# Performance work log

Hardware: AMD Instinct MI355X
Metric: run time of the kernel (lower is better)

## Reference

```python
import jax, jax.numpy as jnp
import numpy as np

N_CELL, N_WELL = 200000, 512
E_CC, E_CW = 1600000, 65536
CF, WF, ED, H = 12, 8, 1, 64
NEG_SLOPE = 0.2


def _p(k, shape, fan_in):
    return jax.random.normal(k, shape, jnp.float32) * (1.0 / np.sqrt(fan_in))


def setup_inputs() -> dict:
    key = jax.random.key(0)
    ks = jax.random.split(key, 32)
    d = {}
    d['cell_x'] = jax.random.normal(ks[0], (N_CELL, CF), jnp.float32)
    d['well_x'] = jax.random.normal(ks[1], (N_WELL, WF), jnp.float32)
    d['c2c_edge_attr'] = jax.random.normal(ks[2], (E_CC, ED), jnp.float32)
    d['c2c_edge_index'] = jax.random.randint(ks[3], (2, E_CC), 0, N_CELL)
    cw_src = jax.random.randint(ks[4], (E_CW,), 0, N_CELL)
    cw_dst = jax.random.randint(ks[5], (E_CW,), 0, N_WELL)
    d['c2w_edge_index'] = jnp.stack([cw_src, cw_dst])
    d['W_cell_emb'] = _p(ks[6], (CF, H), CF)
    d['b_cell_emb'] = jnp.zeros((H,), jnp.float32)
    d['W_well_emb'] = _p(ks[7], (WF, H), WF)
    d['b_well_emb'] = jnp.zeros((H,), jnp.float32)
    d['W_edge_emb'] = _p(ks[8], (ED, H), ED)
    d['b_edge_emb'] = jnp.zeros((H,), jnp.float32)
    d['conv_lin'] = _p(ks[9], (3, H, H), H)
    d['conv_lin_edge'] = _p(ks[10], (3, H, H), H)
    d['conv_att_src'] = _p(ks[11], (3, H), H)
    d['conv_att_dst'] = _p(ks[12], (3, H), H)
    d['conv_att_edge'] = _p(ks[13], (3, H), H)
    d['conv_bias'] = jnp.zeros((3, H), jnp.float32)
    d['wc_lin'] = _p(ks[14], (H, H), H)
    d['wc_att_src'] = _p(ks[15], (H,), H)
    d['wc_att_dst'] = _p(ks[16], (H,), H)
    d['wc_bias'] = jnp.zeros((H,), jnp.float32)
    d['mlp_W1'] = _p(ks[17], (H, H), H)
    d['mlp_b1'] = jnp.zeros((H,), jnp.float32)
    d['mlp_W2'] = _p(ks[18], (H, 75), H)
    d['mlp_b2'] = jnp.zeros((75,), jnp.float32)
    return d


def segment_softmax(logits, seg, num_segments):
    m = jax.ops.segment_max(logits, seg, num_segments=num_segments)
    m = jnp.where(jnp.isfinite(m), m, 0.0)  # empty segments -> 0
    e = jnp.exp(logits - m[seg])
    s = jax.ops.segment_sum(e, seg, num_segments=num_segments)
    return e / s[seg]


def gat_layer(h_src, h_dst, src, dst, lin, att_s, att_d, bias, num_dst,
              edge_feat=None, lin_edge=None, att_e=None):
    # PyG GATConv, heads=1, concat=False, add_self_loops=False
    hs = h_src @ lin                      # [Ns, H]
    hd = hs if h_dst is h_src else h_dst @ lin
    alpha = (hs @ att_s)[src] + (hd @ att_d)[dst]  # [E]
    if edge_feat is not None:
        alpha = alpha + (edge_feat @ lin_edge) @ att_e
    alpha = jax.nn.leaky_relu(alpha, NEG_SLOPE)
    p = segment_softmax(alpha, dst, num_dst)       # scatter-softmax per dst
    out = jax.ops.segment_sum(hs[src] * p[:, None], dst, num_segments=num_dst)
    return out + bias


def reference(cell_x, well_x, c2c_edge_attr,
              W_cell_emb, b_cell_emb, W_well_emb, b_well_emb,
              W_edge_emb, b_edge_emb,
              conv_lin, conv_lin_edge, conv_att_src, conv_att_dst,
              conv_att_edge, conv_bias,
              wc_lin, wc_att_src, wc_att_dst, wc_bias,
              mlp_W1, mlp_b1, mlp_W2, mlp_b2,
              c2c_edge_index, c2w_edge_index):
    h_c = cell_x @ W_cell_emb + b_cell_emb
    h_w = well_x @ W_well_emb + b_well_emb
    ea = c2c_edge_attr @ W_edge_emb + b_edge_emb
    src, dst = c2c_edge_index[0], c2c_edge_index[1]
    n_cell = h_c.shape[0]
    for l in range(3):
        h_c = jax.nn.relu(
            gat_layer(h_c, h_c, src, dst, conv_lin[l], conv_att_src[l],
                      conv_att_dst[l], conv_bias[l], n_cell,
                      edge_feat=ea, lin_edge=conv_lin_edge[l],
                      att_e=conv_att_edge[l]))
    ws, wd = c2w_edge_index[0], c2w_edge_index[1]
    h_well = gat_layer(h_c, h_w, ws, wd, wc_lin, wc_att_src, wc_att_dst,
                       wc_bias, h_w.shape[0])
    out = jax.nn.relu(h_well @ mlp_W1 + mlp_b1) @ mlp_W2 + mlp_b2
    return out.reshape(-1, 3, 25)
```

## Files before the change

### kernel.cpp

```cpp
#include <hip/hip_runtime.h>
#include <hip/hip_fp16.h>
#include <math.h>

#define CCAP 32
#define OVF_CAP 8192

typedef __attribute__((ext_vector_type(8))) _Float16 f16x8;
typedef __attribute__((ext_vector_type(4))) float f32x4;

__device__ __forceinline__ float wsum(float v){
  #pragma unroll
  for (int o=32;o;o>>=1) v += __shfl_xor(v,o);
  return v;
}

__global__ void k_edge_scalars(const float* __restrict__ lin_edge,
                               const float* __restrict__ att_e,
                               const float* __restrict__ Wrow,
                               const float* __restrict__ bemb,
                               float* __restrict__ escal){
  int l = threadIdx.x >> 6, j = threadIdx.x & 63;
  float v = 0.f;
  for (int k=0;k<64;++k) v = fmaf(lin_edge[l*4096 + j*64 + k], att_e[l*64+k], v);
  float sv = wsum(Wrow[j]*v);
  float ov = wsum(bemb[j]*v);
  if (j==0){ escal[l]=sv; escal[3+l]=ov; }
}

__global__ void k_prepA(const float* __restrict__ W_cell, const float* __restrict__ b_cell,
                        const float* __restrict__ lin0, float* __restrict__ weff){
  int t = threadIdx.x;
  for (int o=t; o<832; o+=256){
    float acc = 0.f;
    if (o < 768){
      int r = o >> 6, c2 = o & 63;
      for (int c=0;c<64;++c) acc = fmaf(W_cell[r*64+c], lin0[c*64+c2], acc);
    } else {
      int c2 = o - 768;
      for (int c=0;c<64;++c) acc = fmaf(b_cell[c], lin0[c*64+c2], acc);
    }
    weff[o] = acc;
  }
}

__global__ void k_prepB(const float* __restrict__ W_well, const float* __restrict__ b_well,
                        const float* __restrict__ wc_lin, const float* __restrict__ att_d,
                        float* __restrict__ wprep){
  __shared__ float tmp[64];
  int t = threadIdx.x;
  if (t < 64){
    float a = 0.f;
    for (int c=0;c<64;++c) a = fmaf(wc_lin[t*64+c], att_d[c], a);
    tmp[t] = a;
  }
  __syncthreads();
  if (t < 9){
    float a = 0.f;
    if (t < 8){ for (int k=0;k<64;++k) a = fmaf(W_well[t*64+k], tmp[k], a); }
    else      { for (int k=0;k<64;++k) a = fmaf(b_well[k],     tmp[k], a); }
    wprep[t] = a;
  }
}

__global__ void k_build_cc(const int* __restrict__ src, const int* __restrict__ dst,
                           const float* __restrict__ attr, int* __restrict__ deg,
                           int2* __restrict__ slot, int4* __restrict__ ovf,
                           int* __restrict__ n_ovf, int e){
  int stride = gridDim.x*blockDim.x;
  for (int i = blockIdx.x*blockDim.x + threadIdx.x; i < e; i += stride){
    int d = dst[i];
    int off = atomicAdd(&deg[d], 1);
    if (off < CCAP){
      slot[(d<<5) + off] = make_int2(src[i], __float_as_int(attr[i]));
    } else {
      int x = atomicAdd(n_ovf, 1);
      if (x < OVF_CAP) ovf[x] = make_int4(d, src[i], __float_as_int(attr[i]), 0);
    }
  }
}

__global__ void k_count_w(const int* __restrict__ dst, int* __restrict__ deg,
                          int* __restrict__ off, int e){
  int i = blockIdx.x*blockDim.x + threadIdx.x;
  if (i<e) off[i] = atomicAdd(&deg[dst[i]], 1);
}

__global__ void k_scan_single(const int* __restrict__ deg, int* __restrict__ rowptr, int n){
  __shared__ int sm[1024];
  int t = threadIdx.x;
  sm[t] = (t<n) ? deg[t] : 0; __syncthreads();
  for (int o=1;o<blockDim.x;o<<=1){
    int v = (t>=o)?sm[t-o]:0; __syncthreads();
    sm[t]+=v; __syncthreads();
  }
  if (t<n) rowptr[t+1]=sm[t];
  if (t==0) rowptr[0]=0;
}

__global__ void k_fill_w(const int* __restrict__ src, const int* __restrict__ dst,
                         const int* __restrict__ rowptr, const int* __restrict__ off,
                         int* __restrict__ slot, int e){
  int i = blockIdx.x*blockDim.x + threadIdx.x;
  if (i>=e) return;
  int d = dst[i];
  slot[rowptr[d] + off[i]] = src[i];
}

__global__ __launch_bounds__(256) void k_gemm64m(
    const __half* __restrict__ h, const float* __restrict__ W,
    const float* __restrict__ att_s, const float* __restrict__ att_d,
    __half* __restrict__ hs, float* __restrict__ as_, float* __restrict__ ad_, int n){
  __shared__ _Float16 hT[64][72];
  __shared__ _Float16 wT[64][72];
  int t = threadIdx.x;
  int n0 = blockIdx.x * 64;
  for (int i=t; i<1024; i+=256){
    int k = i >> 4, f4 = (i & 15) << 2;
    float4 w4 = *(const float4*)&W[k*64 + f4];
    wT[f4+0][k] = (_Float16)w4.x;
    wT[f4+1][k] = (_Float16)w4.y;
    wT[f4+2][k] = (_Float16)w4.z;
    wT[f4+3][k] = (_Float16)w4.w;
  }
  for (int i=t; i<512; i+=256){
    int node = i >> 3, c8 = (i & 7) << 3;
    int gn = n0 + node;
    if (gn < n){
      *(f16x8*)&hT[node][c8] = *(const f16x8*)&h[(size_t)gn*64 + c8];
    } else {
      f16x8 z = {0,0,0,0,0,0,0,0};
      *(f16x8*)&hT[node][c8] = z;
    }
  }
  __syncthreads();
  int w = t >> 6, lane = t & 63;
  int lr = lane & 15, lg = lane >> 4;
  f32x4 acc[4];
  #pragma unroll
  for (int c=0;c<4;++c) acc[c] = (f32x4){0.f,0.f,0.f,0.f};
  #pragma unroll
  for (int kk=0; kk<2; ++kk){
    f16x8 a = *(const f16x8*)&hT[16*w + lr][kk*32 + lg*8];
    #pragma unroll
    for (int c=0;c<4;++c){
      f16x8 b = *(const f16x8*)&wT[16*c + lr][kk*32 + lg*8];
      acc[c] = __builtin_amdgcn_mfma_f32_16x16x32_f16(a, b, acc[c], 0, 0, 0);
    }
  }
  float s_att[4], d_att[4];
  #pragma unroll
  for (int c=0;c<4;++c){ s_att[c]=att_s[16*c+lr]; d_att[c]=att_d[16*c+lr]; }
  #pragma unroll
  for (int r=0;r<4;++r){
    int gn = n0 + 16*w + lg*4 + r;
    float sv=0.f, dv=0.f;
    if (gn < n){
      #pragma unroll
      for (int c=0;c<4;++c){
        float v = acc[c][r];
        hs[(size_t)gn*64 + 16*c + lr] = __float2half(v);
        sv = fmaf(v, s_att[c], sv);
        dv = fmaf(v, d_att[c], dv);
      }
    }
    #pragma unroll
    for (int o=8;o;o>>=1){ sv += __shfl_xor(sv,o,16); dv += __shfl_xor(dv,o,16); }
    if (gn < n && lr==0){ as_[gn]=sv; ad_[gn]=dv; }
  }
}

__global__ __launch_bounds__(256) void k_gemm_l0m(
    const float* __restrict__ x, const float* __restrict__ weff,
    const float* __restrict__ att_s, const float* __restrict__ att_d,
    __half* __restrict__ hs, float* __restrict__ as_, float* __restrict__ ad_, int n){
  __shared__ _Float16 xT[64][40];
  __shared__ _Float16 wT[64][40];
  int t = threadIdx.x;
  int n0 = blockIdx.x * 64;
  for (int i=t; i<768; i+=256){
    int node = i / 12, r = i - node*12;
    int gn = n0 + node;
    xT[node][r] = (gn < n) ? (_Float16)x[(size_t)gn*12 + r] : (_Float16)0.f;
  }
  for (int i=t; i<1280; i+=256){
    int node = i / 20, r = 12 + (i % 20);
    xT[node][r] = (_Float16)0.f;
  }
  for (int i=t; i<768; i+=256){
    int k = i >> 6, f = i & 63;
    wT[f][k] = (_Float16)weff[i];
  }
  for (int i=t; i<1280; i+=256){
    int f = i / 20, k = 12 + (i % 20);
    wT[f][k] = (_Float16)0.f;
  }
  __syncthreads();
  int w = t >> 6, lane = t & 63;
  int lr = lane & 15, lg = lane >> 4;
  f32x4 acc[4];
  f16x8 a = *(const f16x8*)&xT[16*w + lr][lg*8];
  #pragma unroll
  for (int c=0;c<4;++c){
    f16x8 b = *(const f16x8*)&wT[16*c + lr][lg*8];
    acc[c] = __builtin_amdgcn_mfma_f32_16x16x32_f16(a, b, (f32x4){0.f,0.f,0.f,0.f}, 0, 0, 0);
  }
  float s_att[4], d_att[4], be[4];
  #pragma unroll
  for (int c=0;c<4;++c){
    s_att[c]=att_s[16*c+lr]; d_att[c]=att_d[16*c+lr]; be[c]=weff[768 + 16*c + lr];
  }
  #pragma unroll
  for (int r=0;r<4;++r){
    int gn = n0 + 16*w + lg*4 + r;
    float sv=0.f, dv=0.f;
    if (gn < n){
      #pragma unroll
      for (int c=0;c<4;++c){
        float v = acc[c][r] + be[c];
        hs[(size_t)gn*64 + 16*c + lr] = __float2half(v);
        sv = fmaf(v, s_att[c], sv);
        dv = fmaf(v, d_att[c], dv);
      }
    }
    #pragma unroll
    for (int o=8;o;o>>=1){ sv += __shfl_xor(sv,o,16); dv += __shfl_xor(dv,o,16); }
    if (gn < n && lr==0){ as_[gn]=sv; ad_[gn]=dv; }
  }
}

template<bool RELU>
__global__ __launch_bounds__(256) void k_gat_agg3(
    const int* __restrict__ deg, const int2* __restrict__ slot,
    const int4* __restrict__ ovf, const int* __restrict__ n_ovf_p,
    const float* __restrict__ as_, const float* __restrict__ ad_,
    const __half* __restrict__ hs, const float* __restrict__ bias,
    const float* __restrict__ escal, int l,
    __half* __restrict__ out, int n){
  int t = threadIdx.x;
  int g = t & 15;
  int node = blockIdx.x*16 + (t >> 4);
  if (node >= n) return;
  int degn = deg[node];
  float4 b4 = *(const float4*)&bias[g*4];
  if (degn == 0){
    float4 r = b4;
    if (RELU){ r.x=fmaxf(r.x,0.f); r.y=fmaxf(r.y,0.f); r.z=fmaxf(r.z,0.f); r.w=fmaxf(r.w,0.f); }
    union { __half2 h2[2]; int2 i2; } u;
    u.h2[0] = __floats2half2_rn(r.x, r.y);
    u.h2[1] = __floats2half2_rn(r.z, r.w);
    *(int2*)&out[(size_t)node*64 + g*4] = u.i2;
    return;
  }
  float se = escal[l], oe = escal[3+l];
  float adn = ad_[node];
  int cin = min(degn, CCAP);
  int sb = node << 5;
  float areg[2]; int sreg[2];
  float m = -1e30f;
  #pragma unroll
  for (int it=0; it<2; ++it){
    int k = it*16 + g;
    areg[it] = -1e30f; sreg[it] = 0;
    if (k < cin){
      int2 sv = slot[sb + k];
      float a = as_[sv.x] + adn;
      a = fmaf(__int_as_float(sv.y), se, a) + oe;
      a = (a >= 0.f) ? a : 0.2f*a;
      areg[it] = a; sreg[it] = sv.x;
      m = fmaxf(m, a);
    }
  }
  int no = 0;
  if (degn > CCAP) no = min(*n_ovf_p, OVF_CAP);
  for (int j=0;j<no;++j){
    int4 e = ovf[j];
    if (e.x == node){
      float a = as_[e.y] + adn;
      a = fmaf(__int_as_float(e.z), se, a) + oe;
      a = (a >= 0.f) ? a : 0.2f*a;
      m = fmaxf(m, a);
    }
  }
  #pragma unroll
  for (int o=8;o;o>>=1) m = fmaxf(m, __shfl_xor(m, o, 16));

  float sum = 0.f;
  float4 acc = make_float4(0.f,0.f,0.f,0.f);
  #pragma unroll
  for (int it=0; it<2; ++it){
    int base = it*16;
    if (base < cin){
      float p = (base + g < cin) ? __expf(areg[it] - m) : 0.f;
      sum += p;
      int cnt = min(16, cin - base);
      for (int j=0;j<cnt;j+=8){
        float pj[8]; int sj[8];
        int s0 = __shfl(sreg[it], j, 16);
        #pragma unroll
        for (int u=0;u<8;++u){
          int jj = j+u;
          bool act = (jj < cnt);
          pj[u] = act ? __shfl(p, jj, 16) : 0.f;
          int sv = __shfl(sreg[it], act ? jj : j, 16);
          sj[u] = act ? sv : s0;
        }
        int2 hb[8];
        #pragma unroll
        for (int u=0;u<8;++u) hb[u] = *(const int2*)&hs[(size_t)sj[u]*64 + g*4];
        #pragma unroll
        for (int u=0;u<8;++u){
          union { unsigned u32; __half2 h2; } a0, a1;
          a0.u32 = (unsigned)hb[u].x; a1.u32 = (unsigned)hb[u].y;
          float2 f0 = __half22float2(a0.h2);
          float2 f1 = __half22float2(a1.h2);
          acc.x = fmaf(f0.x, pj[u], acc.x);
          acc.y = fmaf(f0.y, pj[u], acc.y);
          acc.z = fmaf(f1.x, pj[u], acc.z);
          acc.w = fmaf(f1.y, pj[u], acc.w);
        }
      }
    }
  }
  for (int j=0;j<no;++j){
    int4 e = ovf[j];
    if (e.x == node){
      float a = as_[e.y] + adn;
      a = fmaf(__int_as_float(e.z), se, a) + oe;
      a = (a >= 0.f) ? a : 0.2f*a;
      float p = __expf(a - m);
      if (g == 0) sum += p;
      int2 hb = *(const int2*)&hs[(size_t)e.y*64 + g*4];
      union { unsigned u; __half2 h2; } a0, a1; a0.u = (unsigned)hb.x; a1.u = (unsigned)hb.y;
      float2 f0 = __half22float2(a0.h2);
      float2 f1 = __half22float2(a1.h2);
      acc.x = fmaf(f0.x, p, acc.x);
      acc.y = fmaf(f0.y, p, acc.y);
      acc.z = fmaf(f1.x, p, acc.z);
      acc.w = fmaf(f1.y, p, acc.w);
    }
  }
  #pragma unroll
  for (int o=8;o;o>>=1) sum += __shfl_xor(sum, o, 16);
  float4 r;
  r.x = acc.x/sum + b4.x;
  r.y = acc.y/sum + b4.y;
  r.z = acc.z/sum + b4.z;
  r.w = acc.w/sum + b4.w;
  if (RELU){ r.x=fmaxf(r.x,0.f); r.y=fmaxf(r.y,0.f); r.z=fmaxf(r.z,0.f); r.w=fmaxf(r.w,0.f); }
  union { __half2 h2[2]; int2 i2; } u;
  u.h2[0] = __floats2half2_rn(r.x, r.y);
  u.h2[1] = __floats2half2_rn(r.z, r.w);
  *(int2*)&out[(size_t)node*64 + g*4] = u.i2;
}

template<int NA>
__global__ __launch_bounds__(256) void k_gat_aggw(
    const int* __restrict__ rowptr, const int* __restrict__ slot1,
    float* __restrict__ alpha_ws,
    const float* __restrict__ as_, const float* __restrict__ well_x,
    const float* __restrict__ wprep,
    const __half* __restrict__ hs, const float* __restrict__ bias,
    float* __restrict__ out, int n){
  int t = threadIdx.x;
  int g = t & 15;
  int node = blockIdx.x*16 + (t >> 4);
  if (node >= n) return;
  int beg = rowptr[node], end = rowptr[node+1];
  float4 b4 = *(const float4*)&bias[g*4];
  if (end == beg){
    *(float4*)&out[(size_t)node*64 + g*4] = b4;
    return;
  }
  float adn = wprep[8];
  #pragma unroll
  for (int r=0;r<8;++r) adn = fmaf(well_x[node*8+r], wprep[r], adn);
  float areg[NA]; int sreg[NA];
  float m = -1e30f;
  #pragma unroll
  for (int it=0; it<NA; ++it){
    int k = beg + it*16 + g;
    areg[it] = -1e30f; sreg[it] = 0;
    if (k < end){
      int s = slot1[k];
      float a = as_[s] + adn;
      a = (a >= 0.f) ? a : 0.2f*a;
      areg[it] = a; sreg[it] = s;
      m = fmaxf(m, a);
    }
  }
  for (int k = beg + NA*16 + g; k < end; k += 16){
    int s = slot1[k];
    float a = as_[s] + adn;
    a = (a >= 0.f) ? a : 0.2f*a;
    alpha_ws[k] = a;
    m = fmaxf(m, a);
  }
  #pragma unroll
  for (int o=8;o;o>>=1) m = fmaxf(m, __shfl_xor(m, o, 16));

  float sum = 0.f;
  float4 acc = make_float4(0.f,0.f,0.f,0.f);
  #pragma unroll
  for (int it=0; it<NA; ++it){
    int base = beg + it*16;
    if (base < end){
      float p = (base + g < end) ? __expf(areg[it] - m) : 0.f;
      sum += p;
      int cnt = min(16, end - base);
      for (int j=0;j<cnt;++j){
        float pj = __shfl(p, j, 16);
        int   sj = __shfl(sreg[it], j, 16);
        int2 hb = *(const int2*)&hs[(size_t)sj*64 + g*4];
        union { unsigned u; __half2 h2; } a0, a1; a0.u = (unsigned)hb.x; a1.u = (unsigned)hb.y;
        float2 f0 = __half22float2(a0.h2);
        float2 f1 = __half22float2(a1.h2);
        acc.x = fmaf(f0.x, pj, acc.x);
        acc.y = fmaf(f0.y, pj, acc.y);
        acc.z = fmaf(f1.x, pj, acc.z);
        acc.w = fmaf(f1.y, pj, acc.w);
      }
    }
  }
  for (int base = beg + NA*16; base < end; base += 16){
    int k = base + g;
    float p = 0.f; int s = 0;
    if (k < end){ s = slot1[k]; p = __expf(alpha_ws[k] - m); }
    sum += p;
    int cnt = min(16, end - base);
    for (int j=0;j<cnt;++j){
      float pj = __shfl(p, j, 16);
      int   sj = __shfl(s, j, 16);
      int2 hb = *(const int2*)&hs[(size_t)sj*64 + g*4];
      union { unsigned u; __half2 h2; } a0, a1; a0.u = (unsigned)hb.x; a1.u = (unsigned)hb.y;
      float2 f0 = __half22float2(a0.h2);
      float2 f1 = __half22float2(a1.h2);
      acc.x = fmaf(f0.x, pj, acc.x);
      acc.y = fmaf(f0.y, pj, acc.y);
      acc.z = fmaf(f1.x, pj, acc.z);
      acc.w = fmaf(f1.y, pj, acc.w);
    }
  }
  #pragma unroll
  for (int o=8;o;o>>=1) sum += __shfl_xor(sum, o, 16);
  float4 r;
  r.x = acc.x/sum + b4.x;
  r.y = acc.y/sum + b4.y;
  r.z = acc.z/sum + b4.z;
  r.w = acc.w/sum + b4.w;
  *(float4*)&out[(size_t)node*64 + g*4] = r;
}

__global__ __launch_bounds__(128) void k_mlp(const float* __restrict__ h_well,
    const float* __restrict__ W1, const float* __restrict__ b1,
    const float* __restrict__ W2, const float* __restrict__ b2,
    float* __restrict__ out, int n){
  __shared__ float hr[64]; __shared__ float h1[64];
  int w = blockIdx.x, t = threadIdx.x;
  if (t<64) hr[t] = h_well[w*64+t];
  __syncthreads();
  if (t<64){
    float a = b1[t];
    for (int k=0;k<64;++k) a = fmaf(hr[k], W1[k*64+t], a);
    h1[t] = fmaxf(a, 0.f);
  }
  __syncthreads();
  if (t<75){
    float a = b2[t];
    for (int k=0;k<64;++k) a = fmaf(h1[k], W2[k*75+t], a);
    out[w*75+t] = a;
  }
}

extern "C" void kernel_launch(void* const* d_in, const int* in_sizes, int n_in,
                              void* d_out, int out_size, void* d_ws, size_t ws_size,
                              hipStream_t stream){
  const float* cell_x = (const float*)d_in[0];
  const float* well_x = (const float*)d_in[1];
  const float* eattr  = (const float*)d_in[2];
  const int*   cc_idx = (const int*)d_in[3];
  const int*   cw_idx = (const int*)d_in[4];
  const float* W_cell = (const float*)d_in[5];
  const float* b_cell = (const float*)d_in[6];
  const float* W_well = (const float*)d_in[7];
  const float* b_well = (const float*)d_in[8];
  const float* W_edge = (const float*)d_in[9];
  const float* b_edge = (const float*)d_in[10];
  const float* conv_lin = (const float*)d_in[11];
  const float* conv_lin_edge = (const float*)d_in[12];
  const float* att_src = (const float*)d_in[13];
  const float* att_dst = (const float*)d_in[14];
  const float* att_edge = (const float*)d_in[15];
  const float* conv_bias = (const float*)d_in[16];
  const float* wc_lin = (const float*)d_in[17];
  const float* wc_att_src = (const float*)d_in[18];
  const float* wc_att_dst = (const float*)d_in[19];
  const float* wc_bias = (const float*)d_in[20];
  const float* mlp_W1 = (const float*)d_in[21];
  const float* mlp_b1 = (const float*)d_in[22];
  const float* mlp_W2 = (const float*)d_in[23];
  const float* mlp_b2 = (const float*)d_in[24];

  int n_cell = in_sizes[0]/12;
  int n_well = in_sizes[1]/8;
  int e_cc = in_sizes[2];
  int e_cw = in_sizes[4]/2;

  const int* cc_src = cc_idx;
  const int* cc_dst = cc_idx + e_cc;
  const int* cw_src = cw_idx;
  const int* cw_dst = cw_idx + e_cw;

  char* p = (char*)d_ws;
  auto alloc = [&](size_t bytes)->void*{
    void* r = (void*)p;
    p += (bytes + 255) & ~(size_t)255;
    return r;
  };
  __half* h_cur = (__half*)alloc((size_t)n_cell*64*2);
  __half* hs   = (__half*)alloc((size_t)n_cell*64*2);
  float* as_   = (float*)alloc((size_t)n_cell*4);
  float* ad_   = (float*)alloc((size_t)n_cell*4);
  int* deg     = (int*)alloc((size_t)n_cell*4);
  int2* slot2  = (int2*)alloc((size_t)n_cell*CCAP*8);
  int4* ovf    = (int4*)alloc((size_t)OVF_CAP*16);
  int* n_ovf   = (int*)alloc(256);
  int* wdeg    = (int*)alloc((size_t)n_well*4);
  int* wrowptr = (int*)alloc((size_t)(n_well+1)*4);
  int* woff    = (int*)alloc((size_t)e_cw*4);
  int* wslot   = (int*)alloc((size_t)e_cw*4);
  float* walpha= (float*)alloc((size_t)e_cw*4);
  float* h_well= (float*)alloc((size_t)n_well*64*4);
  float* escal = (float*)alloc(64);
  float* weff  = (float*)alloc(832*4);
  float* wprep = (float*)alloc(16*4);

  hipMemsetAsync(deg, 0, (size_t)n_cell*4, stream);
  hipMemsetAsync(wdeg, 0, (size_t)n_well*4, stream);
  hipMemsetAsync(n_ovf, 0, 4, stream);

  k_edge_scalars<<<1, 192, 0, stream>>>(conv_lin_edge, att_edge, W_edge, b_edge, escal);
  k_prepA<<<1, 256, 0, stream>>>(W_cell, b_cell, conv_lin, weff);
  k_prepB<<<1, 128, 0, stream>>>(W_well, b_well, wc_lin, wc_att_dst, wprep);

  int gB = (e_cc + 255)/256; if (gB > 2048) gB = 2048;
  k_build_cc<<<gB, 256, 0, stream>>>(cc_src, cc_dst, eattr, deg, slot2, ovf, n_ovf, e_cc);

  k_count_w<<<(e_cw+255)/256, 256, 0, stream>>>(cw_dst, wdeg, woff, e_cw);
  k_scan_single<<<1, 512, 0, stream>>>(wdeg, wrowptr, n_well);
  k_fill_w<<<(e_cw+255)/256, 256, 0, stream>>>(cw_src, cw_dst, wrowptr, woff, wslot, e_cw);

  k_gemm_l0m<<<(n_cell+63)/64, 256, 0, stream>>>(cell_x, weff,
      att_src, att_dst, hs, as_, ad_, n_cell);
  k_gat_agg3<true><<<(n_cell+15)/16, 256, 0, stream>>>(deg, slot2, ovf, n_ovf,
      as_, ad_, hs, conv_bias, escal, 0, h_cur, n_cell);

  for (int l=1;l<3;++l){
    k_gemm64m<<<(n_cell+63)/64, 256, 0, stream>>>(h_cur, conv_lin + l*4096,
        att_src + l*64, att_dst + l*64, hs, as_, ad_, n_cell);
    k_gat_agg3<true><<<(n_cell+15)/16, 256, 0, stream>>>(deg, slot2, ovf, n_ovf,
        as_, ad_, hs, conv_bias + l*64, escal, l, h_cur, n_cell);
  }

  k_gemm64m<<<(n_cell+63)/64, 256, 0, stream>>>(h_cur, wc_lin, wc_att_src, wc_att_dst,
      hs, as_, ad_, n_cell);
  k_gat_aggw<16><<<(n_well+15)/16, 256, 0, stream>>>(wrowptr, wslot,
      walpha, as_, well_x, wprep, hs, wc_bias, h_well, n_well);

  k_mlp<<<n_well, 128, 0, stream>>>(h_well, mlp_W1, mlp_b1, mlp_W2, mlp_b2, (float*)d_out, n_well);
}
```

Baseline: 525.4 us.

## Fuse GAT aggregation with next layer's linear transform via LDS tile

Each cell-layer aggregation kernel now processes 64 destination nodes per block, writes the ReLU'd fp16 result into shared memory, then runs the next layer's 64x64 MFMA GEMM and attention dot products in the same kernel. This drops the separate GEMM launches and the global write/read of the intermediate h_cur array. Ping-pong hs/as/ad buffers avoid read-write hazards across layers. In exchange, the gather phase now runs four passes per block with a larger shared-memory footprint and a barrier before the GEMM, which may reduce occupancy and latency hiding in the memory-bound gather.

```diff
diff --git a/kernel.cpp b/kernel.cpp
--- a/kernel.cpp
+++ b/kernel.cpp
@@ -106,69 +106,6 @@
   slot[rowptr[d] + off[i]] = src[i];
 }
 
-__global__ __launch_bounds__(256) void k_gemm64m(
-    const __half* __restrict__ h, const float* __restrict__ W,
-    const float* __restrict__ att_s, const float* __restrict__ att_d,
-    __half* __restrict__ hs, float* __restrict__ as_, float* __restrict__ ad_, int n){
-  __shared__ _Float16 hT[64][72];
-  __shared__ _Float16 wT[64][72];
-  int t = threadIdx.x;
-  int n0 = blockIdx.x * 64;
-  for (int i=t; i<1024; i+=256){
-    int k = i >> 4, f4 = (i & 15) << 2;
-    float4 w4 = *(const float4*)&W[k*64 + f4];
-    wT[f4+0][k] = (_Float16)w4.x;
-    wT[f4+1][k] = (_Float16)w4.y;
-    wT[f4+2][k] = (_Float16)w4.z;
-    wT[f4+3][k] = (_Float16)w4.w;
-  }
-  for (int i=t; i<512; i+=256){
-    int node = i >> 3, c8 = (i & 7) << 3;
-    int gn = n0 + node;
-    if (gn < n){
-      *(f16x8*)&hT[node][c8] = *(const f16x8*)&h[(size_t)gn*64 + c8];
-    } else {
-      f16x8 z = {0,0,0,0,0,0,0,0};
-      *(f16x8*)&hT[node][c8] = z;
-    }
-  }
-  __syncthreads();
-  int w = t >> 6, lane = t & 63;
-  int lr = lane & 15, lg = lane >> 4;
-  f32x4 acc[4];
-  #pragma unroll
-  for (int c=0;c<4;++c) acc[c] = (f32x4){0.f,0.f,0.f,0.f};
-  #pragma unroll
-  for (int kk=0; kk<2; ++kk){
-    f16x8 a = *(const f16x8*)&hT[16*w + lr][kk*32 + lg*8];
-    #pragma unroll
-    for (int c=0;c<4;++c){
-      f16x8 b = *(const f16x8*)&wT[16*c + lr][kk*32 + lg*8];
-      acc[c] = __builtin_amdgcn_mfma_f32_16x16x32_f16(a, b, acc[c], 0, 0, 0);
-    }
-  }
-  float s_att[4], d_att[4];
-  #pragma unroll
-  for (int c=0;c<4;++c){ s_att[c]=att_s[16*c+lr]; d_att[c]=att_d[16*c+lr]; }
-  #pragma unroll
-  for (int r=0;r<4;++r){
-    int gn = n0 + 16*w + lg*4 + r;
-    float sv=0.f, dv=0.f;
-    if (gn < n){
-      #pragma unroll
-      for (int c=0;c<4;++c){
-        float v = acc[c][r];
-        hs[(size_t)gn*64 + 16*c + lr] = __float2half(v);
-        sv = fmaf(v, s_att[c], sv);
-        dv = fmaf(v, d_att[c], dv);
-      }
-    }
-    #pragma unroll
-    for (int o=8;o;o>>=1){ sv += __shfl_xor(sv,o,16); dv += __shfl_xor(dv,o,16); }
-    if (gn < n && lr==0){ as_[gn]=sv; ad_[gn]=dv; }
-  }
-}
-
 __global__ __launch_bounds__(256) void k_gemm_l0m(
     const float* __restrict__ x, const float* __restrict__ weff,
     const float* __restrict__ att_s, const float* __restrict__ att_d,
@@ -228,129 +165,177 @@
   }
 }
 
-template<bool RELU>
-__global__ __launch_bounds__(256) void k_gat_agg3(
+__global__ __launch_bounds__(256) void k_aggm(
     const int* __restrict__ deg, const int2* __restrict__ slot,
     const int4* __restrict__ ovf, const int* __restrict__ n_ovf_p,
-    const float* __restrict__ as_, const float* __restrict__ ad_,
-    const __half* __restrict__ hs, const float* __restrict__ bias,
+    const float* __restrict__ as_p, const float* __restrict__ ad_p,
+    const __half* __restrict__ hs_prev, const float* __restrict__ bias,
     const float* __restrict__ escal, int l,
-    __half* __restrict__ out, int n){
+    const float* __restrict__ W, const float* __restrict__ att_s,
+    const float* __restrict__ att_d,
+    __half* __restrict__ hs_next, float* __restrict__ as_o,
+    float* __restrict__ ad_o, int n){
+  __shared__ _Float16 hT[64][72];
+  __shared__ _Float16 wT[64][72];
   int t = threadIdx.x;
-  int g = t & 15;
-  int node = blockIdx.x*16 + (t >> 4);
-  if (node >= n) return;
-  int degn = deg[node];
+  int n0 = blockIdx.x * 64;
+  for (int i=t; i<1024; i+=256){
+    int k = i >> 4, f4 = (i & 15) << 2;
+    float4 w4 = *(const float4*)&W[k*64 + f4];
+    wT[f4+0][k] = (_Float16)w4.x;
+    wT[f4+1][k] = (_Float16)w4.y;
+    wT[f4+2][k] = (_Float16)w4.z;
+    wT[f4+3][k] = (_Float16)w4.w;
+  }
+  int g = t & 15, g16 = t >> 4;
+  float se = escal[l], oe = escal[3+l];
   float4 b4 = *(const float4*)&bias[g*4];
-  if (degn == 0){
-    float4 r = b4;
-    if (RELU){ r.x=fmaxf(r.x,0.f); r.y=fmaxf(r.y,0.f); r.z=fmaxf(r.z,0.f); r.w=fmaxf(r.w,0.f); }
+  #pragma unroll
+  for (int pass=0; pass<4; ++pass){
+    int nl = pass*16 + g16;
+    int node = n0 + nl;
+    float4 r;
+    if (node >= n){
+      r = make_float4(0.f,0.f,0.f,0.f);
+    } else {
+      int degn = deg[node];
+      if (degn == 0){
+        r.x=fmaxf(b4.x,0.f); r.y=fmaxf(b4.y,0.f); r.z=fmaxf(b4.z,0.f); r.w=fmaxf(b4.w,0.f);
+      } else {
+        float adn = ad_p[node];
+        int cin = min(degn, CCAP);
+        int sb = node << 5;
+        float areg[2]; int sreg[2];
+        float m = -1e30f;
+        #pragma unroll
+        for (int it=0; it<2; ++it){
+          int k = it*16 + g;
+          areg[it] = -1e30f; sreg[it] = 0;
+          if (k < cin){
+            int2 sv = slot[sb + k];
+            float a = as_p[sv.x] + adn;
+            a = fmaf(__int_as_float(sv.y), se, a) + oe;
+            a = (a >= 0.f) ? a : 0.2f*a;
+            areg[it] = a; sreg[it] = sv.x;
+            m = fmaxf(m, a);
+          }
+        }
+        int no = 0;
+        if (degn > CCAP) no = min(*n_ovf_p, OVF_CAP);
+        for (int j=0;j<no;++j){
+          int4 e = ovf[j];
+          if (e.x == node){
+            float a = as_p[e.y] + adn;
+            a = fmaf(__int_as_float(e.z), se, a) + oe;
+            a = (a >= 0.f) ? a : 0.2f*a;
+            m = fmaxf(m, a);
+          }
+        }
+        #pragma unroll
+        for (int o=8;o;o>>=1) m = fmaxf(m, __shfl_xor(m, o, 16));
+        float sum = 0.f;
+        float4 acc = make_float4(0.f,0.f,0.f,0.f);
+        #pragma unroll
+        for (int it=0; it<2; ++it){
+          int base = it*16;
+          if (base < cin){
+            float p = (base + g < cin) ? __expf(areg[it] - m) : 0.f;
+            sum += p;
+            int cnt = min(16, cin - base);
+            for (int j=0;j<cnt;j+=8){
+              float pj[8]; int sj[8];
+              int s0 = __shfl(sreg[it], j, 16);
+              #pragma unroll
+              for (int u=0;u<8;++u){
+                int jj = j+u;
+                bool act = (jj < cnt);
+                pj[u] = act ? __shfl(p, jj, 16) : 0.f;
+                int sv = __shfl(sreg[it], act ? jj : j, 16);
+                sj[u] = act ? sv : s0;
+              }
+              int2 hb[8];
+              #pragma unroll
+              for (int u=0;u<8;++u) hb[u] = *(const int2*)&hs_prev[(size_t)sj[u]*64 + g*4];
+              #pragma unroll
+              for (int u=0;u<8;++u){
+                union { unsigned u32; __half2 h2; } a0, a1;
+                a0.u32 = (unsigned)hb[u].x; a1.u32 = (unsigned)hb[u].y;
+                float2 f0 = __half22float2(a0.h2);
+                float2 f1 = __half22float2(a1.h2);
+                acc.x = fmaf(f0.x, pj[u], acc.x);
+                acc.y = fmaf(f0.y, pj[u], acc.y);
+                acc.z = fmaf(f1.x, pj[u], acc.z);
+                acc.w = fmaf(f1.y, pj[u], acc.w);
+              }
+            }
+          }
+        }
+        for (int j=0;j<no;++j){
+          int4 e = ovf[j];
+          if (e.x == node){
+            float a = as_p[e.y] + adn;
+            a = fmaf(__int_as_float(e.z), se, a) + oe;
+            a = (a >= 0.f) ? a : 0.2f*a;
+            float p = __expf(a - m);
+            if (g == 0) sum += p;
+            int2 hb = *(const int2*)&hs_prev[(size_t)e.y*64 + g*4];
+            union { unsigned u; __half2 h2; } a0, a1; a0.u = (unsigned)hb.x; a1.u = (unsigned)hb.y;
+            float2 f0 = __half22float2(a0.h2);
+            float2 f1 = __half22float2(a1.h2);
+            acc.x = fmaf(f0.x, p, acc.x);
+            acc.y = fmaf(f0.y, p, acc.y);
+            acc.z = fmaf(f1.x, p, acc.z);
+            acc.w = fmaf(f1.y, p, acc.w);
+          }
+        }
+        #pragma unroll
+        for (int o=8;o;o>>=1) sum += __shfl_xor(sum, o, 16);
+        r.x = fmaxf(acc.x/sum + b4.x, 0.f);
+        r.y = fmaxf(acc.y/sum + b4.y, 0.f);
+        r.z = fmaxf(acc.z/sum + b4.z, 0.f);
+        r.w = fmaxf(acc.w/sum + b4.w, 0.f);
+      }
+    }
     union { __half2 h2[2]; int2 i2; } u;
     u.h2[0] = __floats2half2_rn(r.x, r.y);
     u.h2[1] = __floats2half2_rn(r.z, r.w);
-    *(int2*)&out[(size_t)node*64 + g*4] = u.i2;
-    return;
-  }
-  float se = escal[l], oe = escal[3+l];
-  float adn = ad_[node];
-  int cin = min(degn, CCAP);
-  int sb = node << 5;
-  float areg[2]; int sreg[2];
-  float m = -1e30f;
-  #pragma unroll
-  for (int it=0; it<2; ++it){
-    int k = it*16 + g;
-    areg[it] = -1e30f; sreg[it] = 0;
-    if (k < cin){
-      int2 sv = slot[sb + k];
-      float a = as_[sv.x] + adn;
-      a = fmaf(__int_as_float(sv.y), se, a) + oe;
-      a = (a >= 0.f) ? a : 0.2f*a;
-      areg[it] = a; sreg[it] = sv.x;
-      m = fmaxf(m, a);
-    }
-  }
-  int no = 0;
-  if (degn > CCAP) no = min(*n_ovf_p, OVF_CAP);
-  for (int j=0;j<no;++j){
-    int4 e = ovf[j];
-    if (e.x == node){
-      float a = as_[e.y] + adn;
-      a = fmaf(__int_as_float(e.z), se, a) + oe;
-      a = (a >= 0.f) ? a : 0.2f*a;
-      m = fmaxf(m, a);
-    }
-  }
-  #pragma unroll
-  for (int o=8;o;o>>=1) m = fmaxf(m, __shfl_xor(m, o, 16));
-
-  float sum = 0.f;
-  float4 acc = make_float4(0.f,0.f,0.f,0.f);
-  #pragma unroll
-  for (int it=0; it<2; ++it){
-    int base = it*16;
-    if (base < cin){
-      float p = (base + g < cin) ? __expf(areg[it] - m) : 0.f;
-      sum += p;
-      int cnt = min(16, cin - base);
-      for (int j=0;j<cnt;j+=8){
-        float pj[8]; int sj[8];
-        int s0 = __shfl(sreg[it], j, 16);
-        #pragma unroll
-        for (int u=0;u<8;++u){
-          int jj = j+u;
-          bool act = (jj < cnt);
-          pj[u] = act ? __shfl(p, jj, 16) : 0.f;
-          int sv = __shfl(sreg[it], act ? jj : j, 16);
-          sj[u] = act ? sv : s0;
-        }
-        int2 hb[8];
-        #pragma unroll
-        for (int u=0;u<8;++u) hb[u] = *(const int2*)&hs[(size_t)sj[u]*64 + g*4];
-        #pragma unroll
-        for (int u=0;u<8;++u){
-          union { unsigned u32; __half2 h2; } a0, a1;
-          a0.u32 = (unsigned)hb[u].x; a1.u32 = (unsigned)hb[u].y;
-          float2 f0 = __half22float2(a0.h2);
-          float2 f1 = __half22float2(a1.h2);
-          acc.x = fmaf(f0.x, pj[u], acc.x);
-          acc.y = fmaf(f0.y, pj[u], acc.y);
-          acc.z = fmaf(f1.x, pj[u], acc.z);
-          acc.w = fmaf(f1.y, pj[u], acc.w);
-        }
+    *(int2*)&hT[nl][g*4] = u.i2;
+  }
+  __syncthreads();
+  int w = t >> 6, lane = t & 63;
+  int lr = lane & 15, lg = lane >> 4;
+  f32x4 acc2[4];
+  #pragma unroll
+  for (int c=0;c<4;++c) acc2[c] = (f32x4){0.f,0.f,0.f,0.f};
+  #pragma unroll
+  for (int kk=0; kk<2; ++kk){
+    f16x8 a = *(const f16x8*)&hT[16*w + lr][kk*32 + lg*8];
+    #pragma unroll
+    for (int c=0;c<4;++c){
+      f16x8 b = *(const f16x8*)&wT[16*c + lr][kk*32 + lg*8];
+      acc2[c] = __builtin_amdgcn_mfma_f32_16x16x32_f16(a, b, acc2[c], 0, 0, 0);
+    }
+  }
+  float s_att[4], d_att[4];
+  #pragma unroll
+  for (int c=0;c<4;++c){ s_att[c]=att_s[16*c+lr]; d_att[c]=att_d[16*c+lr]; }
+  #pragma unroll
+  for (int r=0;r<4;++r){
+    int gn = n0 + 16*w + lg*4 + r;
+    float sv=0.f, dv=0.f;
+    if (gn < n){
+      #pragma unroll
+      for (int c=0;c<4;++c){
+        float v = acc2[c][r];
+        hs_next[(size_t)gn*64 + 16*c + lr] = __float2half(v);
+        sv = fmaf(v, s_att[c], sv);
+        dv = fmaf(v, d_att[c], dv);
       }
     }
-  }
-  for (int j=0;j<no;++j){
-    int4 e = ovf[j];
-    if (e.x == node){
-      float a = as_[e.y] + adn;
-      a = fmaf(__int_as_float(e.z), se, a) + oe;
-      a = (a >= 0.f) ? a : 0.2f*a;
-      float p = __expf(a - m);
-      if (g == 0) sum += p;
-      int2 hb = *(const int2*)&hs[(size_t)e.y*64 + g*4];
-      union { unsigned u; __half2 h2; } a0, a1; a0.u = (unsigned)hb.x; a1.u = (unsigned)hb.y;
-      float2 f0 = __half22float2(a0.h2);
-      float2 f1 = __half22float2(a1.h2);
-      acc.x = fmaf(f0.x, p, acc.x);
-      acc.y = fmaf(f0.y, p, acc.y);
-      acc.z = fmaf(f1.x, p, acc.z);
-      acc.w = fmaf(f1.y, p, acc.w);
-    }
-  }
-  #pragma unroll
-  for (int o=8;o;o>>=1) sum += __shfl_xor(sum, o, 16);
-  float4 r;
-  r.x = acc.x/sum + b4.x;
-  r.y = acc.y/sum + b4.y;
-  r.z = acc.z/sum + b4.z;
-  r.w = acc.w/sum + b4.w;
-  if (RELU){ r.x=fmaxf(r.x,0.f); r.y=fmaxf(r.y,0.f); r.z=fmaxf(r.z,0.f); r.w=fmaxf(r.w,0.f); }
-  union { __half2 h2[2]; int2 i2; } u;
-  u.h2[0] = __floats2half2_rn(r.x, r.y);
-  u.h2[1] = __floats2half2_rn(r.z, r.w);
-  *(int2*)&out[(size_t)node*64 + g*4] = u.i2;
+    #pragma unroll
+    for (int o=8;o;o>>=1){ sv += __shfl_xor(sv,o,16); dv += __shfl_xor(dv,o,16); }
+    if (gn < n && lr==0){ as_o[gn]=sv; ad_o[gn]=dv; }
+  }
 }
 
 template<int NA>
@@ -516,10 +501,12 @@
     p += (bytes + 255) & ~(size_t)255;
     return r;
   };
-  __half* h_cur = (__half*)alloc((size_t)n_cell*64*2);
-  __half* hs   = (__half*)alloc((size_t)n_cell*64*2);
-  float* as_   = (float*)alloc((size_t)n_cell*4);
-  float* ad_   = (float*)alloc((size_t)n_cell*4);
+  __half* hsA  = (__half*)alloc((size_t)n_cell*64*2);
+  __half* hsB  = (__half*)alloc((size_t)n_cell*64*2);
+  float* asA   = (float*)alloc((size_t)n_cell*4);
+  float* adA   = (float*)alloc((size_t)n_cell*4);
+  float* asB   = (float*)alloc((size_t)n_cell*4);
+  float* adB   = (float*)alloc((size_t)n_cell*4);
   int* deg     = (int*)alloc((size_t)n_cell*4);
   int2* slot2  = (int2*)alloc((size_t)n_cell*CCAP*8);
   int4* ovf    = (int4*)alloc((size_t)OVF_CAP*16);
@@ -549,22 +536,22 @@
   k_scan_single<<<1, 512, 0, stream>>>(wdeg, wrowptr, n_well);
   k_fill_w<<<(e_cw+255)/256, 256, 0, stream>>>(cw_src, cw_dst, wrowptr, woff, wslot, e_cw);
 
-  k_gemm_l0m<<<(n_cell+63)/64, 256, 0, stream>>>(cell_x, weff,
-      att_src, att_dst, hs, as_, ad_, n_cell);
-  k_gat_agg3<true><<<(n_cell+15)/16, 256, 0, stream>>>(deg, slot2, ovf, n_ovf,
-      as_, ad_, hs, conv_bias, escal, 0, h_cur, n_cell);
-
-  for (int l=1;l<3;++l){
-    k_gemm64m<<<(n_cell+63)/64, 256, 0, stream>>>(h_cur, conv_lin + l*4096,
-        att_src + l*64, att_dst + l*64, hs, as_, ad_, n_cell);
-    k_gat_agg3<true><<<(n_cell+15)/16, 256, 0, stream>>>(deg, slot2, ovf, n_ovf,
-        as_, ad_, hs, conv_bias + l*64, escal, l, h_cur, n_cell);
-  }
-
-  k_gemm64m<<<(n_cell+63)/64, 256, 0, stream>>>(h_cur, wc_lin, wc_att_src, wc_att_dst,
-      hs, as_, ad_, n_cell);
+  int gN = (n_cell+63)/64;
+
+  k_gemm_l0m<<<gN, 256, 0, stream>>>(cell_x, weff, att_src, att_dst,
+      hsA, asA, adA, n_cell);
+
+  k_aggm<<<gN, 256, 0, stream>>>(deg, slot2, ovf, n_ovf, asA, adA, hsA,
+      conv_bias, escal, 0, conv_lin + 4096, att_src + 64, att_dst + 64,
+      hsB, asB, adB, n_cell);
+  k_aggm<<<gN, 256, 0, stream>>>(deg, slot2, ovf, n_ovf, asB, adB, hsB,
+      conv_bias + 64, escal, 1, conv_lin + 8192, att_src + 128, att_dst + 128,
+      hsA, asA, adA, n_cell);
+  k_aggm<<<gN, 256, 0, stream>>>(deg, slot2, ovf, n_ovf, asA, adA, hsA,
+      conv_bias + 128, escal, 2, wc_lin, wc_att_src, wc_att_dst,
+      hsB, asB, adB, n_cell);
+
   k_gat_aggw<16><<<(n_well+15)/16, 256, 0, stream>>>(wrowptr, wslot,
-      walpha, as_, well_x, wprep, hs, wc_bias, h_well, n_well);
-
+      walpha, asB, well_x, wprep, hsB, wc_bias, h_well, n_well);
   k_mlp<<<n_well, 128, 0, stream>>>(h_well, mlp_W1, mlp_b1, mlp_W2, mlp_b2, (float*)d_out, n_well);
 }
```

Result: no change. 528.8 us (+0.7%).
